# Kernel optimization log

Measured on AMD Instinct MI355X. Metric: run time of the kernel, lower is better.

## Reference

```python
import jax, jax.numpy as jnp
import numpy as np

N_NODES = 100000
N_EDGES = 1600000
D_FEAT = 64
NUM_LAYERS = 4  # -> num_gcn_layers = 3


def spmm(edge_row, edge_col, edge_vals, x, n_nodes):
    # out[r] = sum_{e: row[e]==r} vals[e] * x[col[e]]
    gathered = edge_vals[:, None] * x[edge_col]  # [E, d]
    return jax.ops.segment_sum(gathered, edge_row, num_segments=n_nodes)


def setup_inputs() -> dict:
    key = jax.random.key(0)
    k1, k2, k3, k4 = jax.random.split(key, 4)
    x = jax.random.normal(k1, (N_NODES, D_FEAT), dtype=jnp.float32)
    edge_row = jax.random.randint(k2, (N_EDGES,), 0, N_NODES, dtype=jnp.int32)
    edge_col = jax.random.randint(k3, (N_EDGES,), 0, N_NODES, dtype=jnp.int32)
    edge_vals = jax.random.uniform(k4, (N_EDGES,), dtype=jnp.float32)
    return {"x": x, "edge_row": edge_row, "edge_col": edge_col, "edge_vals": edge_vals}


def reference(x, edge_row, edge_col, edge_vals):
    # resSumGCN: h_{i+1} = A h_i ; return sum_{i=1..L} h_i
    num_gcn_layers = NUM_LAYERS - 1
    h = x
    acc = jnp.zeros_like(x)
    for _ in range(num_gcn_layers):  # small fixed layer count
        h = spmm(edge_row, edge_col, edge_vals, h, N_NODES)
        acc = acc + h
    return acc
```

## Files before the change

kernel.cpp:

```cpp
#include <hip/hip_runtime.h>

#define N_NODES 100000
#define N_EDGES 1600000
#define D_FEAT  64

#define RSHIFT 8
#define RPB    256
#define NBK    ((N_NODES + RPB - 1) / RPB)
#define CAP    5120
#define EPB    4096
#define KBLK   ((N_EDGES + EPB - 1) / EPB)
#define OROW   (NBK + 1)
#define CVB    ((N_NODES * D_FEAT / 4 + 1023) / 1024)

typedef float f32x2 __attribute__((ext_vector_type(2)));

__device__ __forceinline__ unsigned short f2bf(float f) {
  union { float f; unsigned int i; } v; v.f = f;
  unsigned int b = v.i;
  return (unsigned short)((b + 0x7FFFu + ((b >> 16) & 1u)) >> 16);
}
__device__ __forceinline__ float ulo(int u) { return __int_as_float(u << 16); }
__device__ __forceinline__ float uhi(int u) { return __int_as_float(u & 0xFFFF0000); }
__device__ __forceinline__ f32x2 upk(int u) {
  f32x2 r; r.x = ulo(u); r.y = uhi(u); return r;
}
__device__ __forceinline__ int pk(float a, float b) {
  return (int)f2bf(a) | ((int)f2bf(b) << 16);
}

__global__ __launch_bounds__(1024) void convert_bin(
    const float4* __restrict__ xin, ushort4* __restrict__ xout,
    const int* __restrict__ erow, const int* __restrict__ ecol,
    const float* __restrict__ evals, int2* __restrict__ tmp,
    int* __restrict__ offs) {
  __shared__ int hist[NBK];
  __shared__ int sc[NBK];
  int t = threadIdx.x;
  int k = blockIdx.x;
  if (k >= KBLK) {
    int i = (k - KBLK) * 1024 + t;
    if (i < N_NODES * D_FEAT / 4) {
      float4 v = xin[i];
      ushort4 o;
      o.x = f2bf(v.x); o.y = f2bf(v.y); o.z = f2bf(v.z); o.w = f2bf(v.w);
      xout[i] = o;
    }
    return;
  }
  if (t < NBK) hist[t] = 0;
  __syncthreads();
  int base = k * EPB;
  int nk = N_EDGES - base; if (nk > EPB) nk = EPB;
  int key[4], vb[4], rk[4], bk[4];
#pragma unroll
  for (int j = 0; j < 4; ++j) {
    int li = j * 1024 + t;
    bk[j] = -1;
    if (li < nk) {
      int e = base + li;
      int r = erow[e];
      key[j] = ((r & (RPB - 1)) << 17) | ecol[e];
      vb[j]  = __float_as_int(evals[e]);
      bk[j]  = r >> RSHIFT;
      rk[j]  = atomicAdd(&hist[bk[j]], 1);
    }
  }
  __syncthreads();
  if (t < NBK) sc[t] = hist[t];
  __syncthreads();
  for (int off = 1; off < NBK; off <<= 1) {
    int u = (t >= off && t < NBK) ? sc[t - off] : 0;
    __syncthreads();
    if (t < NBK) sc[t] += u;
    __syncthreads();
  }
  if (t < NBK) {
    int ex = sc[t] - hist[t];
    sc[t] = ex;
    offs[k * OROW + t] = ex;
  }
  if (t == 0) offs[k * OROW + NBK] = nk;
  __syncthreads();
#pragma unroll
  for (int j = 0; j < 4; ++j) {
    if (bk[j] >= 0) {
      int pos = sc[bk[j]] + rk[j];
      tmp[k * EPB + pos] = make_int2(key[j], vb[j]);
    }
  }
}

__global__ __launch_bounds__(256) void build_csr(
    const int2* __restrict__ tmp, const int* __restrict__ offs,
    int2* __restrict__ edges, int* __restrict__ row_beg,
    int* __restrict__ row_end) {
  __shared__ int hist[RPB];
  __shared__ int cur[RPB];
  int b = blockIdx.x;
  int t = threadIdx.x;
  int oct = t >> 3;
  int ol  = t & 7;
  hist[t] = 0;
  __syncthreads();
  for (int k = oct; k < KBLK; k += 32) {
    int o0 = offs[k * OROW + b];
    int o1 = offs[k * OROW + b + 1];
    const int2* seg = tmp + k * EPB;
    for (int i = o0 + ol; i < o1; i += 8)
      atomicAdd(&hist[seg[i].x >> 17], 1);
  }
  __syncthreads();
  int v  = hist[t];
  int v2 = (v + 1) & ~1;
  cur[t] = v2;
  __syncthreads();
  for (int off = 1; off < 256; off <<= 1) {
    int u = (t >= off) ? cur[t - off] : 0;
    __syncthreads();
    cur[t] += u;
    __syncthreads();
  }
  int excl2 = cur[t] - v2;
  int base = b * CAP;
  int gr = b * RPB + t;
  if (gr < N_NODES) {
    row_beg[gr] = base + excl2;
    row_end[gr] = base + excl2 + v;
  }
  if (v & 1) edges[base + excl2 + v] = make_int2(0, 0);
  __syncthreads();
  cur[t] = excl2;
  __syncthreads();
  for (int k = oct; k < KBLK; k += 32) {
    int o0 = offs[k * OROW + b];
    int o1 = offs[k * OROW + b + 1];
    const int2* seg = tmp + k * EPB;
    for (int i = o0 + ol; i < o1; i += 8) {
      int2 ed = seg[i];
      int pos = atomicAdd(&cur[ed.x >> 17], 1);
      edges[base + pos] = make_int2(ed.x & 0x1FFFF, ed.y);
    }
  }
}

__global__ __launch_bounds__(256) void spmm_oct(
    const int* __restrict__ row_beg, const int* __restrict__ row_end,
    const int2* __restrict__ edges, const int4* __restrict__ xq,
    int4* __restrict__ h_q, float4* __restrict__ out,
    const int4* __restrict__ add1, const int4* __restrict__ add2,
    int final_mode) {
  int t = threadIdx.x;
  int lane = t & 63;
  int oct = lane >> 3;
  int ol  = lane & 7;
  int row = blockIdx.x * 32 + (t >> 6) * 8 + oct;
  int e0 = row_beg[row];
  int e1 = row_end[row];
  const int4* ep = (const int4*)edges + (e0 >> 1);
  int npair = (e1 - e0 + 1) >> 1;
  f32x2 c0 = {0.f, 0.f}, c1 = {0.f, 0.f}, c2 = {0.f, 0.f}, c3 = {0.f, 0.f};

#define PAIR(m) { \
    int4 g0 = xq[(size_t)(m).x * 8 + ol]; \
    int4 g1 = xq[(size_t)(m).z * 8 + ol]; \
    float v0 = __int_as_float((m).y), v1 = __int_as_float((m).w); \
    f32x2 vv0 = {v0, v0}, vv1 = {v1, v1}; \
    c0 += vv0 * upk(g0.x) + vv1 * upk(g1.x); \
    c1 += vv0 * upk(g0.y) + vv1 * upk(g1.y); \
    c2 += vv0 * upk(g0.z) + vv1 * upk(g1.z); \
    c3 += vv0 * upk(g0.w) + vv1 * upk(g1.w); \
  }

  int p = 0;
  for (; p + 2 <= npair; p += 2) {
    int4 m0 = ep[p];
    int4 m1 = ep[p + 1];
    PAIR(m0);
    PAIR(m1);
  }
  if (p < npair) {
    int4 m0 = ep[p];
    PAIR(m0);
  }
#undef PAIR

  size_t oi = (size_t)row * 8 + ol;
  if (final_mode) {
    int4 r1 = add1[oi];
    int4 r2 = add2[oi];
    float4 lo, hi;
    lo.x = c0.x + ulo(r1.x) + ulo(r2.x);
    lo.y = c0.y + uhi(r1.x) + uhi(r2.x);
    lo.z = c1.x + ulo(r1.y) + ulo(r2.y);
    lo.w = c1.y + uhi(r1.y) + uhi(r2.y);
    hi.x = c2.x + ulo(r1.z) + ulo(r2.z);
    hi.y = c2.y + uhi(r1.z) + uhi(r2.z);
    hi.z = c3.x + ulo(r1.w) + ulo(r2.w);
    hi.w = c3.y + uhi(r1.w) + uhi(r2.w);
    out[(size_t)row * 16 + ol * 2]     = lo;
    out[(size_t)row * 16 + ol * 2 + 1] = hi;
  } else {
    int4 pq;
    pq.x = pk(c0.x, c0.y);
    pq.y = pk(c1.x, c1.y);
    pq.z = pk(c2.x, c2.y);
    pq.w = pk(c3.x, c3.y);
    h_q[oi] = pq;
  }
}

extern "C" void kernel_launch(void* const* d_in, const int* in_sizes, int n_in,
                              void* d_out, int out_size, void* d_ws, size_t ws_size,
                              hipStream_t stream) {
  const float* x     = (const float*)d_in[0];
  const int*   erow  = (const int*)d_in[1];
  const int*   ecol  = (const int*)d_in[2];
  const float* evals = (const float*)d_in[3];
  float* out = (float*)d_out;

  const size_t hb_bytes   = (size_t)N_NODES * D_FEAT * 2;
  const size_t ecap_bytes = (size_t)NBK * CAP * sizeof(int2);
  char* ws = (char*)d_ws;
  int4*    xbf  = (int4*)   (ws);
  int4*    bufA = (int4*)   (ws + hb_bytes);
  int2*    tmp  = (int2*)   (ws + hb_bytes);
  int4*    bufB = (int4*)   (ws + 2 * hb_bytes);
  int*     offs = (int*)    (ws + 2 * hb_bytes);
  int2* edges   = (int2*)(ws + 3 * hb_bytes);
  int* row_beg  = (int*) (ws + 3 * hb_bytes + ecap_bytes);
  int* row_end  = (int*) (ws + 3 * hb_bytes + ecap_bytes + 400000);

  const int sblocks = N_NODES / 32;

  convert_bin<<<KBLK + CVB, 1024, 0, stream>>>(
      (const float4*)x, (ushort4*)xbf, erow, ecol, evals, tmp, offs);
  build_csr<<<NBK, 256, 0, stream>>>(tmp, offs, edges, row_beg, row_end);

  spmm_oct<<<sblocks, 256, 0, stream>>>(row_beg, row_end, edges, xbf,
                                        bufA, nullptr, nullptr, nullptr, 0);
  spmm_oct<<<sblocks, 256, 0, stream>>>(row_beg, row_end, edges, bufA,
                                        bufB, nullptr, nullptr, nullptr, 0);
  spmm_oct<<<sblocks, 256, 0, stream>>>(row_beg, row_end, edges, bufB,
                                        nullptr, (float4*)out, bufA, bufB, 1);
}
```

Baseline: 226.1 us.

## Sort rows by degree bin so SpMM wavefronts process equal-length rows

```diff
diff --git a/kernel.cpp b/kernel.cpp
--- a/kernel.cpp
+++ b/kernel.cpp
@@ -12,6 +12,7 @@
 #define KBLK   ((N_EDGES + EPB - 1) / EPB)
 #define OROW   (NBK + 1)
 #define CVB    ((N_NODES * D_FEAT / 4 + 1023) / 1024)
+#define NPBIN  64
 
 typedef float f32x2 __attribute__((ext_vector_type(2)));
 
@@ -33,11 +34,12 @@
     const float4* __restrict__ xin, ushort4* __restrict__ xout,
     const int* __restrict__ erow, const int* __restrict__ ecol,
     const float* __restrict__ evals, int2* __restrict__ tmp,
-    int* __restrict__ offs) {
+    int* __restrict__ offs, int* __restrict__ dhist) {
   __shared__ int hist[NBK];
   __shared__ int sc[NBK];
   int t = threadIdx.x;
   int k = blockIdx.x;
+  if (k == 0 && t < NPBIN) dhist[t] = 0;
   if (k >= KBLK) {
     int i = (k - KBLK) * 1024 + t;
     if (i < N_NODES * D_FEAT / 4) {
@@ -94,14 +96,16 @@
 __global__ __launch_bounds__(256) void build_csr(
     const int2* __restrict__ tmp, const int* __restrict__ offs,
     int2* __restrict__ edges, int* __restrict__ row_beg,
-    int* __restrict__ row_end) {
+    int* __restrict__ row_end, int* __restrict__ dhist) {
   __shared__ int hist[RPB];
   __shared__ int cur[RPB];
+  __shared__ int dh[NPBIN];
   int b = blockIdx.x;
   int t = threadIdx.x;
   int oct = t >> 3;
   int ol  = t & 7;
   hist[t] = 0;
+  if (t < NPBIN) dh[t] = 0;
   __syncthreads();
   for (int k = oct; k < KBLK; k += 32) {
     int o0 = offs[k * OROW + b];
@@ -114,7 +118,14 @@
   int v  = hist[t];
   int v2 = (v + 1) & ~1;
   cur[t] = v2;
-  __syncthreads();
+  int gr = b * RPB + t;
+  {
+    int np  = v2 >> 1;
+    int bin = np > (NPBIN - 1) ? (NPBIN - 1) : np;
+    if (gr < N_NODES) atomicAdd(&dh[bin], 1);
+  }
+  __syncthreads();
+  if (t < NPBIN) { int c = dh[t]; if (c) atomicAdd(&dhist[t], c); }
   for (int off = 1; off < 256; off <<= 1) {
     int u = (t >= off) ? cur[t - off] : 0;
     __syncthreads();
@@ -123,7 +134,6 @@
   }
   int excl2 = cur[t] - v2;
   int base = b * CAP;
-  int gr = b * RPB + t;
   if (gr < N_NODES) {
     row_beg[gr] = base + excl2;
     row_end[gr] = base + excl2 + v;
@@ -144,19 +154,55 @@
   }
 }
 
+__global__ __launch_bounds__(64) void scan64(const int* __restrict__ dhist,
+                                             int* __restrict__ gbase) {
+  int t = threadIdx.x;
+  int v = dhist[t];
+  int s = v;
+  for (int off = 1; off < 64; off <<= 1) {
+    int u = __shfl_up(s, off);
+    if (t >= off) s += u;
+  }
+  gbase[t] = s - v;
+}
+
+__global__ __launch_bounds__(256) void perm_scatter(
+    const int* __restrict__ row_beg, const int* __restrict__ row_end,
+    int* __restrict__ gbase, int4* __restrict__ prows) {
+  __shared__ int lh[NPBIN];
+  __shared__ int lbase[NPBIN];
+  int t = threadIdx.x;
+  int r = blockIdx.x * 256 + t;
+  if (t < NPBIN) lh[t] = 0;
+  __syncthreads();
+  int e0 = 0, e1 = 0, bin = 0, rank = 0;
+  bool valid = r < N_NODES;
+  if (valid) {
+    e0 = row_beg[r];
+    e1 = row_end[r];
+    int np = (e1 - e0 + 1) >> 1;
+    bin = np > (NPBIN - 1) ? (NPBIN - 1) : np;
+    rank = atomicAdd(&lh[bin], 1);
+  }
+  __syncthreads();
+  if (t < NPBIN) { int c = lh[t]; lbase[t] = c ? atomicAdd(&gbase[t], c) : 0; }
+  __syncthreads();
+  if (valid) prows[lbase[bin] + rank] = make_int4(e0, e1, r, 0);
+}
+
 __global__ __launch_bounds__(256) void spmm_oct(
-    const int* __restrict__ row_beg, const int* __restrict__ row_end,
-    const int2* __restrict__ edges, const int4* __restrict__ xq,
-    int4* __restrict__ h_q, float4* __restrict__ out,
-    const int4* __restrict__ add1, const int4* __restrict__ add2,
-    int final_mode) {
+    const int4* __restrict__ prows, const int2* __restrict__ edges,
+    const int4* __restrict__ xq, int4* __restrict__ h_q,
+    float4* __restrict__ out, const int4* __restrict__ add1,
+    const int4* __restrict__ add2, int final_mode) {
   int t = threadIdx.x;
   int lane = t & 63;
   int oct = lane >> 3;
   int ol  = lane & 7;
-  int row = blockIdx.x * 32 + (t >> 6) * 8 + oct;
-  int e0 = row_beg[row];
-  int e1 = row_end[row];
+  int slot = blockIdx.x * 32 + (t >> 6) * 8 + oct;
+  int4 pr = prows[slot];
+  int e0 = pr.x, e1 = pr.y;
+  int row = pr.z;
   const int4* ep = (const int4*)edges + (e0 >> 1);
   int npair = (e1 - e0 + 1) >> 1;
   f32x2 c0 = {0.f, 0.f}, c1 = {0.f, 0.f}, c2 = {0.f, 0.f}, c3 = {0.f, 0.f};
@@ -172,15 +218,23 @@
     c3 += vv0 * upk(g0.w) + vv1 * upk(g1.w); \
   }
 
-  int p = 0;
-  for (; p + 2 <= npair; p += 2) {
-    int4 m0 = ep[p];
-    int4 m1 = ep[p + 1];
+  int np2 = npair & ~1;
+  if (np2) {
+    int4 m0 = ep[0];
+    int4 m1 = ep[1];
+    for (int p = 2; p < np2; p += 2) {
+      int4 n0 = ep[p];
+      int4 n1 = ep[p + 1];
+      PAIR(m0);
+      PAIR(m1);
+      m0 = n0;
+      m1 = n1;
+    }
     PAIR(m0);
     PAIR(m1);
   }
-  if (p < npair) {
-    int4 m0 = ep[p];
+  if (npair & 1) {
+    int4 m0 = ep[npair - 1];
     PAIR(m0);
   }
 #undef PAIR
@@ -230,17 +284,24 @@
   int2* edges   = (int2*)(ws + 3 * hb_bytes);
   int* row_beg  = (int*) (ws + 3 * hb_bytes + ecap_bytes);
   int* row_end  = (int*) (ws + 3 * hb_bytes + ecap_bytes + 400000);
+  char* pext    = ws + 3 * hb_bytes + ecap_bytes + 800000;
+  int4* prows   = (int4*)(pext);
+  int*  dhist   = (int*) (pext + 1600000);
+  int*  gbase   = dhist + NPBIN;
 
   const int sblocks = N_NODES / 32;
+  const int rblocks = (N_NODES + 255) / 256;
 
   convert_bin<<<KBLK + CVB, 1024, 0, stream>>>(
-      (const float4*)x, (ushort4*)xbf, erow, ecol, evals, tmp, offs);
-  build_csr<<<NBK, 256, 0, stream>>>(tmp, offs, edges, row_beg, row_end);
-
-  spmm_oct<<<sblocks, 256, 0, stream>>>(row_beg, row_end, edges, xbf,
+      (const float4*)x, (ushort4*)xbf, erow, ecol, evals, tmp, offs, dhist);
+  build_csr<<<NBK, 256, 0, stream>>>(tmp, offs, edges, row_beg, row_end, dhist);
+  scan64<<<1, 64, 0, stream>>>(dhist, gbase);
+  perm_scatter<<<rblocks, 256, 0, stream>>>(row_beg, row_end, gbase, prows);
+
+  spmm_oct<<<sblocks, 256, 0, stream>>>(prows, edges, xbf,
                                         bufA, nullptr, nullptr, nullptr, 0);
-  spmm_oct<<<sblocks, 256, 0, stream>>>(row_beg, row_end, edges, bufA,
+  spmm_oct<<<sblocks, 256, 0, stream>>>(prows, edges, bufA,
                                         bufB, nullptr, nullptr, nullptr, 0);
-  spmm_oct<<<sblocks, 256, 0, stream>>>(row_beg, row_end, edges, bufB,
+  spmm_oct<<<sblocks, 256, 0, stream>>>(prows, edges, bufB,
                                         nullptr, (float4*)out, bufA, bufB, 1);
 }
```

New measurement: 239.3 us. 5.9% more time.

## Software-pipeline SpMM gathers and double build_csr block threads

Applied to the files above, without the earlier changes.

```diff
diff --git a/kernel.cpp b/kernel.cpp
--- a/kernel.cpp
+++ b/kernel.cpp
@@ -91,7 +91,7 @@
   }
 }
 
-__global__ __launch_bounds__(256) void build_csr(
+__global__ __launch_bounds__(512) void build_csr(
     const int2* __restrict__ tmp, const int* __restrict__ offs,
     int2* __restrict__ edges, int* __restrict__ row_beg,
     int* __restrict__ row_end) {
@@ -101,9 +101,9 @@
   int t = threadIdx.x;
   int oct = t >> 3;
   int ol  = t & 7;
-  hist[t] = 0;
-  __syncthreads();
-  for (int k = oct; k < KBLK; k += 32) {
+  if (t < RPB) hist[t] = 0;
+  __syncthreads();
+  for (int k = oct; k < KBLK; k += 64) {
     int o0 = offs[k * OROW + b];
     int o1 = offs[k * OROW + b + 1];
     const int2* seg = tmp + k * EPB;
@@ -111,28 +111,34 @@
       atomicAdd(&hist[seg[i].x >> 17], 1);
   }
   __syncthreads();
-  int v  = hist[t];
-  int v2 = (v + 1) & ~1;
-  cur[t] = v2;
-  __syncthreads();
-  for (int off = 1; off < 256; off <<= 1) {
-    int u = (t >= off) ? cur[t - off] : 0;
-    __syncthreads();
-    cur[t] += u;
-    __syncthreads();
-  }
-  int excl2 = cur[t] - v2;
+  int v = 0, v2 = 0;
+  if (t < RPB) {
+    v  = hist[t];
+    v2 = (v + 1) & ~1;
+    cur[t] = v2;
+  }
+  __syncthreads();
+  for (int off = 1; off < RPB; off <<= 1) {
+    int u = (t >= off && t < RPB) ? cur[t - off] : 0;
+    __syncthreads();
+    if (t < RPB) cur[t] += u;
+    __syncthreads();
+  }
+  int excl2 = 0;
   int base = b * CAP;
-  int gr = b * RPB + t;
-  if (gr < N_NODES) {
-    row_beg[gr] = base + excl2;
-    row_end[gr] = base + excl2 + v;
-  }
-  if (v & 1) edges[base + excl2 + v] = make_int2(0, 0);
-  __syncthreads();
-  cur[t] = excl2;
-  __syncthreads();
-  for (int k = oct; k < KBLK; k += 32) {
+  if (t < RPB) {
+    excl2 = cur[t] - v2;
+    int gr = b * RPB + t;
+    if (gr < N_NODES) {
+      row_beg[gr] = base + excl2;
+      row_end[gr] = base + excl2 + v;
+    }
+    if (v & 1) edges[base + excl2 + v] = make_int2(0, 0);
+  }
+  __syncthreads();
+  if (t < RPB) cur[t] = excl2;
+  __syncthreads();
+  for (int k = oct; k < KBLK; k += 64) {
     int o0 = offs[k * OROW + b];
     int o1 = offs[k * OROW + b + 1];
     const int2* seg = tmp + k * EPB;
@@ -161,29 +167,66 @@
   int npair = (e1 - e0 + 1) >> 1;
   f32x2 c0 = {0.f, 0.f}, c1 = {0.f, 0.f}, c2 = {0.f, 0.f}, c3 = {0.f, 0.f};
 
-#define PAIR(m) { \
-    int4 g0 = xq[(size_t)(m).x * 8 + ol]; \
-    int4 g1 = xq[(size_t)(m).z * 8 + ol]; \
+#define GATH(g0, g1, m) \
+    g0 = xq[(size_t)(m).x * 8 + ol]; \
+    g1 = xq[(size_t)(m).z * 8 + ol];
+#define FMA_P(g0, g1, m) { \
     float v0 = __int_as_float((m).y), v1 = __int_as_float((m).w); \
     f32x2 vv0 = {v0, v0}, vv1 = {v1, v1}; \
-    c0 += vv0 * upk(g0.x) + vv1 * upk(g1.x); \
-    c1 += vv0 * upk(g0.y) + vv1 * upk(g1.y); \
-    c2 += vv0 * upk(g0.z) + vv1 * upk(g1.z); \
-    c3 += vv0 * upk(g0.w) + vv1 * upk(g1.w); \
-  }
-
-  int p = 0;
-  for (; p + 2 <= npair; p += 2) {
-    int4 m0 = ep[p];
-    int4 m1 = ep[p + 1];
-    PAIR(m0);
-    PAIR(m1);
-  }
-  if (p < npair) {
-    int4 m0 = ep[p];
-    PAIR(m0);
-  }
-#undef PAIR
+    c0 += vv0 * upk((g0).x) + vv1 * upk((g1).x); \
+    c1 += vv0 * upk((g0).y) + vv1 * upk((g1).y); \
+    c2 += vv0 * upk((g0).z) + vv1 * upk((g1).z); \
+    c3 += vv0 * upk((g0).w) + vv1 * upk((g1).w); \
+  }
+
+  if (npair >= 2) {
+    int4 mA0 = ep[0], mA1 = ep[1];
+    int4 a0, a1, a2, a3;
+    GATH(a0, a1, mA0);
+    GATH(a2, a3, mA1);
+    int q = 2;
+    while (q + 4 <= npair) {
+      int4 mB0 = ep[q], mB1 = ep[q + 1];
+      int4 b0, b1, b2, b3;
+      GATH(b0, b1, mB0);
+      GATH(b2, b3, mB1);
+      FMA_P(a0, a1, mA0);
+      FMA_P(a2, a3, mA1);
+      mA0 = ep[q + 2]; mA1 = ep[q + 3];
+      GATH(a0, a1, mA0);
+      GATH(a2, a3, mA1);
+      FMA_P(b0, b1, mB0);
+      FMA_P(b2, b3, mB1);
+      q += 4;
+    }
+    if (q + 2 <= npair) {
+      int4 mB0 = ep[q], mB1 = ep[q + 1];
+      int4 b0, b1, b2, b3;
+      GATH(b0, b1, mB0);
+      GATH(b2, b3, mB1);
+      FMA_P(a0, a1, mA0);
+      FMA_P(a2, a3, mA1);
+      FMA_P(b0, b1, mB0);
+      FMA_P(b2, b3, mB1);
+      q += 2;
+    } else {
+      FMA_P(a0, a1, mA0);
+      FMA_P(a2, a3, mA1);
+    }
+    if (q < npair) {
+      int4 m = ep[q];
+      int4 g0, g1;
+      GATH(g0, g1, m);
+      FMA_P(g0, g1, m);
+    }
+  } else if (npair == 1) {
+    int4 m = ep[0];
+    int4 g0, g1;
+    GATH(g0, g1, m);
+    FMA_P(g0, g1, m);
+  }
+#undef GATH
+#undef FMA_P
 
   size_t oi = (size_t)row * 8 + ol;
   if (final_mode) {
@@ -235,7 +278,7 @@
 
   convert_bin<<<KBLK + CVB, 1024, 0, stream>>>(
       (const float4*)x, (ushort4*)xbf, erow, ecol, evals, tmp, offs);
-  build_csr<<<NBK, 256, 0, stream>>>(tmp, offs, edges, row_beg, row_end);
+  build_csr<<<NBK, 512, 0, stream>>>(tmp, offs, edges, row_beg, row_end);
 
   spmm_oct<<<sblocks, 256, 0, stream>>>(row_beg, row_end, edges, xbf,
                                         bufA, nullptr, nullptr, nullptr, 0);
```

New measurement: 228.0 us. About the same (+0.9%).

## Sort edges within rows by column octant and process two rows per thread

Applied to the files above, without the earlier changes.

```diff
diff --git a/kernel.cpp b/kernel.cpp
--- a/kernel.cpp
+++ b/kernel.cpp
@@ -12,6 +12,8 @@
 #define KBLK   ((N_EDGES + EPB - 1) / EPB)
 #define OROW   (NBK + 1)
 #define CVB    ((N_NODES * D_FEAT / 4 + 1023) / 1024)
+#define NOCT   8
+#define SB2    ((N_NODES + 63) / 64)
 
 typedef float f32x2 __attribute__((ext_vector_type(2)));
 
@@ -91,123 +93,150 @@
   }
 }
 
-__global__ __launch_bounds__(256) void build_csr(
+__global__ __launch_bounds__(512) void build_csr(
     const int2* __restrict__ tmp, const int* __restrict__ offs,
     int2* __restrict__ edges, int* __restrict__ row_beg,
-    int* __restrict__ row_end) {
-  __shared__ int hist[RPB];
-  __shared__ int cur[RPB];
+    int2* __restrict__ cnt8) {
+  __shared__ int hist[RPB * 8];
+  __shared__ int cur[RPB * 8];
+  __shared__ int sc[RPB];
   int b = blockIdx.x;
   int t = threadIdx.x;
-  int oct = t >> 3;
-  int ol  = t & 7;
-  hist[t] = 0;
-  __syncthreads();
-  for (int k = oct; k < KBLK; k += 32) {
+  int o8 = t >> 3;
+  int ol = t & 7;
+  for (int i = t; i < RPB * 8; i += 512) hist[i] = 0;
+  __syncthreads();
+  for (int k = o8; k < KBLK; k += 64) {
     int o0 = offs[k * OROW + b];
     int o1 = offs[k * OROW + b + 1];
     const int2* seg = tmp + k * EPB;
-    for (int i = o0 + ol; i < o1; i += 8)
-      atomicAdd(&hist[seg[i].x >> 17], 1);
-  }
-  __syncthreads();
-  int v  = hist[t];
-  int v2 = (v + 1) & ~1;
-  cur[t] = v2;
-  __syncthreads();
-  for (int off = 1; off < 256; off <<= 1) {
-    int u = (t >= off) ? cur[t - off] : 0;
-    __syncthreads();
-    cur[t] += u;
-    __syncthreads();
-  }
-  int excl2 = cur[t] - v2;
-  int base = b * CAP;
-  int gr = b * RPB + t;
-  if (gr < N_NODES) {
-    row_beg[gr] = base + excl2;
-    row_end[gr] = base + excl2 + v;
-  }
-  if (v & 1) edges[base + excl2 + v] = make_int2(0, 0);
-  __syncthreads();
-  cur[t] = excl2;
-  __syncthreads();
-  for (int k = oct; k < KBLK; k += 32) {
+    for (int i = o0 + ol; i < o1; i += 8) {
+      int key = seg[i].x;
+      atomicAdd(&hist[((key >> 17) << 3) | ((key >> 14) & 7)], 1);
+    }
+  }
+  __syncthreads();
+  int v = 0, v2 = 0;
+  if (t < RPB) {
+#pragma unroll
+    for (int o = 0; o < 8; ++o) v += hist[t * 8 + o];
+    v2 = (v + 1) & ~1;
+    sc[t] = v2;
+  }
+  __syncthreads();
+  for (int off = 1; off < RPB; off <<= 1) {
+    int u = (t >= off && t < RPB) ? sc[t - off] : 0;
+    __syncthreads();
+    if (t < RPB) sc[t] += u;
+    __syncthreads();
+  }
+  if (t < RPB) {
+    int excl2 = sc[t] - v2;
+    int run = excl2;
+    unsigned int lo = 0, hi = 0;
+#pragma unroll
+    for (int o = 0; o < 8; ++o) {
+      cur[t * 8 + o] = run;
+      int c = hist[t * 8 + o];
+      run += c;
+      unsigned int cc = (unsigned)(c > 255 ? 255 : c);
+      if (o < 4) lo |= cc << (8 * o); else hi |= cc << (8 * (o - 4));
+    }
+    int gr = b * RPB + t;
+    if (gr < N_NODES) {
+      row_beg[gr] = b * CAP + excl2;
+      cnt8[gr] = make_int2((int)lo, (int)hi);
+    }
+  }
+  __syncthreads();
+  for (int k = o8; k < KBLK; k += 64) {
     int o0 = offs[k * OROW + b];
     int o1 = offs[k * OROW + b + 1];
     const int2* seg = tmp + k * EPB;
     for (int i = o0 + ol; i < o1; i += 8) {
       int2 ed = seg[i];
-      int pos = atomicAdd(&cur[ed.x >> 17], 1);
-      edges[base + pos] = make_int2(ed.x & 0x1FFFF, ed.y);
-    }
-  }
-}
-
-__global__ __launch_bounds__(256) void spmm_oct(
-    const int* __restrict__ row_beg, const int* __restrict__ row_end,
+      int idx = ((ed.x >> 17) << 3) | ((ed.x >> 14) & 7);
+      int pos = atomicAdd(&cur[idx], 1);
+      edges[b * CAP + pos] = make_int2(ed.x & 0x1FFFF, ed.y);
+    }
+  }
+}
+
+__global__ __launch_bounds__(256, 7) void spmm_pass(
+    const int* __restrict__ row_beg, const int2* __restrict__ cnt8,
     const int2* __restrict__ edges, const int4* __restrict__ xq,
     int4* __restrict__ h_q, float4* __restrict__ out,
     const int4* __restrict__ add1, const int4* __restrict__ add2,
     int final_mode) {
   int t = threadIdx.x;
   int lane = t & 63;
-  int oct = lane >> 3;
-  int ol  = lane & 7;
-  int row = blockIdx.x * 32 + (t >> 6) * 8 + oct;
-  int e0 = row_beg[row];
-  int e1 = row_end[row];
-  const int4* ep = (const int4*)edges + (e0 >> 1);
-  int npair = (e1 - e0 + 1) >> 1;
-  f32x2 c0 = {0.f, 0.f}, c1 = {0.f, 0.f}, c2 = {0.f, 0.f}, c3 = {0.f, 0.f};
-
-#define PAIR(m) { \
-    int4 g0 = xq[(size_t)(m).x * 8 + ol]; \
-    int4 g1 = xq[(size_t)(m).z * 8 + ol]; \
-    float v0 = __int_as_float((m).y), v1 = __int_as_float((m).w); \
-    f32x2 vv0 = {v0, v0}, vv1 = {v1, v1}; \
-    c0 += vv0 * upk(g0.x) + vv1 * upk(g1.x); \
-    c1 += vv0 * upk(g0.y) + vv1 * upk(g1.y); \
-    c2 += vv0 * upk(g0.z) + vv1 * upk(g1.z); \
-    c3 += vv0 * upk(g0.w) + vv1 * upk(g1.w); \
-  }
-
-  int p = 0;
-  for (; p + 2 <= npair; p += 2) {
-    int4 m0 = ep[p];
-    int4 m1 = ep[p + 1];
-    PAIR(m0);
-    PAIR(m1);
-  }
-  if (p < npair) {
-    int4 m0 = ep[p];
-    PAIR(m0);
-  }
-#undef PAIR
-
-  size_t oi = (size_t)row * 8 + ol;
-  if (final_mode) {
-    int4 r1 = add1[oi];
-    int4 r2 = add2[oi];
-    float4 lo, hi;
-    lo.x = c0.x + ulo(r1.x) + ulo(r2.x);
-    lo.y = c0.y + uhi(r1.x) + uhi(r2.x);
-    lo.z = c1.x + ulo(r1.y) + ulo(r2.y);
-    lo.w = c1.y + uhi(r1.y) + uhi(r2.y);
-    hi.x = c2.x + ulo(r1.z) + ulo(r2.z);
-    hi.y = c2.y + uhi(r1.z) + uhi(r2.z);
-    hi.z = c3.x + ulo(r1.w) + ulo(r2.w);
-    hi.w = c3.y + uhi(r1.w) + uhi(r2.w);
-    out[(size_t)row * 16 + ol * 2]     = lo;
-    out[(size_t)row * 16 + ol * 2 + 1] = hi;
-  } else {
-    int4 pq;
-    pq.x = pk(c0.x, c0.y);
-    pq.y = pk(c1.x, c1.y);
-    pq.z = pk(c2.x, c2.y);
-    pq.w = pk(c3.x, c3.y);
-    h_q[oi] = pq;
-  }
+  int oc = lane >> 3;
+  int ol = lane & 7;
+  int w = t >> 6;
+  int r0 = blockIdx.x * 64 + w * 8 + oc;
+  int r1 = r0 + 32;
+  bool val0 = r0 < N_NODES, val1 = r1 < N_NODES;
+  int off0 = 0, off1 = 0;
+  int2 k0 = make_int2(0, 0), k1 = make_int2(0, 0);
+  if (val0) { off0 = row_beg[r0]; k0 = cnt8[r0]; }
+  if (val1) { off1 = row_beg[r1]; k1 = cnt8[r1]; }
+  f32x2 a0 = {0.f,0.f}, a1 = {0.f,0.f}, a2 = {0.f,0.f}, a3 = {0.f,0.f};
+  f32x2 b0 = {0.f,0.f}, b1 = {0.f,0.f}, b2 = {0.f,0.f}, b3 = {0.f,0.f};
+
+#pragma unroll
+  for (int p = 0; p < 7; ++p) {
+    int c0 = ((p < 4 ? (k0.x >> (8 * p)) : (k0.y >> (8 * (p - 4)))) & 255);
+    for (int i = 0; i < c0; ++i) {
+      int2 m = edges[off0 + i];
+      int4 g = xq[(size_t)m.x * 8 + ol];
+      float vv = __int_as_float(m.y);
+      f32x2 vx = {vv, vv};
+      a0 += vx * upk(g.x); a1 += vx * upk(g.y);
+      a2 += vx * upk(g.z); a3 += vx * upk(g.w);
+    }
+    off0 += c0;
+    int c1 = ((p < 4 ? (k1.x >> (8 * p)) : (k1.y >> (8 * (p - 4)))) & 255);
+    for (int i = 0; i < c1; ++i) {
+      int2 m = edges[off1 + i];
+      int4 g = xq[(size_t)m.x * 8 + ol];
+      float vv = __int_as_float(m.y);
+      f32x2 vx = {vv, vv};
+      b0 += vx * upk(g.x); b1 += vx * upk(g.y);
+      b2 += vx * upk(g.z); b3 += vx * upk(g.w);
+    }
+    off1 += c1;
+  }
+
+#define EPILOG(row, valid, c0v, c1v, c2v, c3v) \
+  if (valid) { \
+    size_t oi = (size_t)(row) * 8 + ol; \
+    if (final_mode) { \
+      int4 r1v = add1[oi]; \
+      int4 r2v = add2[oi]; \
+      float4 lo, hi; \
+      lo.x = (c0v).x + ulo(r1v.x) + ulo(r2v.x); \
+      lo.y = (c0v).y + uhi(r1v.x) + uhi(r2v.x); \
+      lo.z = (c1v).x + ulo(r1v.y) + ulo(r2v.y); \
+      lo.w = (c1v).y + uhi(r1v.y) + uhi(r2v.y); \
+      hi.x = (c2v).x + ulo(r1v.z) + ulo(r2v.z); \
+      hi.y = (c2v).y + uhi(r1v.z) + uhi(r2v.z); \
+      hi.z = (c3v).x + ulo(r1v.w) + ulo(r2v.w); \
+      hi.w = (c3v).y + uhi(r1v.w) + uhi(r2v.w); \
+      out[(size_t)(row) * 16 + ol * 2]     = lo; \
+      out[(size_t)(row) * 16 + ol * 2 + 1] = hi; \
+    } else { \
+      int4 pq; \
+      pq.x = pk((c0v).x, (c0v).y); \
+      pq.y = pk((c1v).x, (c1v).y); \
+      pq.z = pk((c2v).x, (c2v).y); \
+      pq.w = pk((c3v).x, (c3v).y); \
+      h_q[oi] = pq; \
+    } \
+  }
+
+  EPILOG(r0, val0, a0, a1, a2, a3)
+  EPILOG(r1, val1, b0, b1, b2, b3)
+#undef EPILOG
 }
 
 extern "C" void kernel_launch(void* const* d_in, const int* in_sizes, int n_in,
@@ -222,25 +251,23 @@
   const size_t hb_bytes   = (size_t)N_NODES * D_FEAT * 2;
   const size_t ecap_bytes = (size_t)NBK * CAP * sizeof(int2);
   char* ws = (char*)d_ws;
-  int4*    xbf  = (int4*)   (ws);
-  int4*    bufA = (int4*)   (ws + hb_bytes);
-  int2*    tmp  = (int2*)   (ws + hb_bytes);
-  int4*    bufB = (int4*)   (ws + 2 * hb_bytes);
-  int*     offs = (int*)    (ws + 2 * hb_bytes);
-  int2* edges   = (int2*)(ws + 3 * hb_bytes);
-  int* row_beg  = (int*) (ws + 3 * hb_bytes + ecap_bytes);
-  int* row_end  = (int*) (ws + 3 * hb_bytes + ecap_bytes + 400000);
-
-  const int sblocks = N_NODES / 32;
+  int4* xbf   = (int4*)(ws);
+  int4* bufA  = (int4*)(ws + hb_bytes);
+  int2* tmp   = (int2*)(ws + hb_bytes);
+  int4* bufB  = (int4*)(ws + 2 * hb_bytes);
+  int*  offs  = (int*) (ws + 2 * hb_bytes);
+  int2* edges = (int2*)(ws + 3 * hb_bytes);
+  int*  row_beg = (int*)(ws + 3 * hb_bytes + ecap_bytes);
+  int2* cnt8    = (int2*)(ws + 3 * hb_bytes + ecap_bytes + 400000);
 
   convert_bin<<<KBLK + CVB, 1024, 0, stream>>>(
       (const float4*)x, (ushort4*)xbf, erow, ecol, evals, tmp, offs);
-  build_csr<<<NBK, 256, 0, stream>>>(tmp, offs, edges, row_beg, row_end);
-
-  spmm_oct<<<sblocks, 256, 0, stream>>>(row_beg, row_end, edges, xbf,
-                                        bufA, nullptr, nullptr, nullptr, 0);
-  spmm_oct<<<sblocks, 256, 0, stream>>>(row_beg, row_end, edges, bufA,
-                                        bufB, nullptr, nullptr, nullptr, 0);
-  spmm_oct<<<sblocks, 256, 0, stream>>>(row_beg, row_end, edges, bufB,
-                                        nullptr, (float4*)out, bufA, bufB, 1);
-}
+  build_csr<<<NBK, 512, 0, stream>>>(tmp, offs, edges, row_beg, cnt8);
+
+  spmm_pass<<<SB2, 256, 0, stream>>>(row_beg, cnt8, edges, xbf,
+                                     bufA, nullptr, nullptr, nullptr, 0);
+  spmm_pass<<<SB2, 256, 0, stream>>>(row_beg, cnt8, edges, bufA,
+                                     bufB, nullptr, nullptr, nullptr, 0);
+  spmm_pass<<<SB2, 256, 0, stream>>>(row_beg, cnt8, edges, bufB,
+                                     nullptr, (float4*)out, bufA, bufB, 1);
+}
```

After: 282.7 us. 1.25x slower.
